# Performance work log

Measured on AMD Instinct MI355X. Metric: run time of the kernel, lower is better.

The kernel has to match this reference:

```python
import jax, jax.numpy as jnp
import numpy as np

HEADS = 8
DIM_HEAD = 64
SCALE = DIM_HEAD ** -0.5


def setup_inputs() -> dict:
    key = jax.random.key(0)
    k1, k2, k3 = jax.random.split(key, 3)
    b, p, n, dim = 2, 16, 512, 512
    inner = HEADS * DIM_HEAD  # 512
    x = jax.random.normal(k1, (b, p, n, dim), dtype=jnp.float32)
    W_qkv = jax.random.normal(k2, (dim, 3 * inner), dtype=jnp.float32) * (dim ** -0.5)
    W_out = jax.random.normal(k3, (inner, dim), dtype=jnp.float32) * (inner ** -0.5)
    b_out = jnp.zeros((dim,), dtype=jnp.float32)
    return {"x": x, "W_qkv": W_qkv, "W_out": W_out, "b_out": b_out}


def reference(x, W_qkv, W_out, b_out):
    b, p, n, dim = x.shape
    # QKV projection (no bias), split into q, k, v
    qkv = jnp.einsum('bpnd,de->bpne', x, W_qkv)
    q, k, v = jnp.split(qkv, 3, axis=-1)
    # (b, p, n, h*d) -> (b, p, h, n, d)
    def to_heads(t):
        return t.reshape(b, p, n, HEADS, DIM_HEAD).transpose(0, 1, 3, 2, 4)
    q, k, v = to_heads(q), to_heads(k), to_heads(v)
    # attention scores: (b, p, h, n, n)
    dots = jnp.einsum('bphnd,bphmd->bphnm', q, k) * SCALE
    attn = jax.nn.softmax(dots, axis=-1)
    out = jnp.einsum('bphnm,bphmd->bphnd', attn, v)
    # (b, p, h, n, d) -> (b, p, n, h*d)
    out = out.transpose(0, 1, 3, 2, 4).reshape(b, p, n, HEADS * DIM_HEAD)
    # output projection (dropout rate = 0.0 -> identity)
    return jnp.einsum('bpne,ed->bpnd', out, W_out) + b_out
```

## Files before the change

### kernel.cpp

```cpp
#include <hip/hip_runtime.h>
#include <hip/hip_bf16.h>

typedef short bf16x8 __attribute__((ext_vector_type(8)));
typedef short bf16x4 __attribute__((ext_vector_type(4)));
typedef float f32x4  __attribute__((ext_vector_type(4)));

__device__ __forceinline__ unsigned short f2bf(float f) {
    union { float fv; unsigned int u; } v; v.fv = f;
    unsigned int r = v.u + 0x7FFFu + ((v.u >> 16) & 1u);
    return (unsigned short)(r >> 16);
}

__device__ __forceinline__ void gload16(const short* g, short* l) {
    __builtin_amdgcn_global_load_lds(
        (const __attribute__((address_space(1))) void*)g,
        (__attribute__((address_space(3))) void*)l, 16, 0, 0);
}

__global__ __launch_bounds__(256) void cvt_x(
    const float* __restrict__ x, short* __restrict__ xb)
{
    size_t i = ((size_t)blockIdx.x * 256 + threadIdx.x) * 8;
    f32x4 a = *(const f32x4*)(x + i);
    f32x4 b = *(const f32x4*)(x + i + 4);
    bf16x8 s;
    #pragma unroll
    for (int e = 0; e < 4; ++e) { s[e] = (short)f2bf(a[e]); s[4 + e] = (short)f2bf(b[e]); }
    *(bf16x8*)(xb + i) = s;
}

__global__ __launch_bounds__(256) void prep_w(
    const float* __restrict__ Wqkv, const float* __restrict__ Wout,
    short* __restrict__ Wqkvt, short* __restrict__ Woutt)
{
    int idx = blockIdx.x * 256 + threadIdx.x;
    int n = idx >> 9, k = idx & 511;
    Wqkvt[idx] = (short)f2bf(Wqkv[(size_t)k * 1536 + n]);
    if (idx < 512 * 512) {
        Woutt[idx] = (short)f2bf(Wout[(size_t)k * 512 + n]);
    }
}

template<int F32OUT>
__global__ __launch_bounds__(256, 2) void gemm_db(
    const short* __restrict__ A, const short* __restrict__ Bt,
    short* __restrict__ Cb, float* __restrict__ Cf, const float* __restrict__ bias,
    int M, int N, int K, int NB)
{
    __shared__ short lds[2][2][128 * 64];
    const int t    = threadIdx.x;
    const int lane = t & 63;
    const int wid  = t >> 6;
    const int l15  = lane & 15;
    const int lg   = lane >> 4;

    const int cpx = gridDim.x >> 3;
    const int swz = (blockIdx.x & 7) * cpx + (blockIdx.x >> 3);
    const int m0 = (swz / NB) * 128;
    const int n0 = (swz % NB) * 128;

    const int wm = (wid >> 1) * 64;
    const int wn = (wid & 1) * 64;

    const int scol = 8 * ((lane & 7) ^ ((lane >> 3) & 7));

    float bval[4];
    if constexpr (F32OUT) {
        #pragma unroll
        for (int ni = 0; ni < 4; ++ni) bval[ni] = bias[n0 + wn + ni * 16 + l15];
    }

    f32x4 acc[4][4];
    #pragma unroll
    for (int i = 0; i < 4; ++i)
        #pragma unroll
        for (int j = 0; j < 4; ++j)
            acc[i][j] = f32x4{0.f, 0.f, 0.f, 0.f};

    const int NT = K >> 6;

    auto stage = [&](int buf, int tk) {
        #pragma unroll
        for (int j = 0; j < 4; ++j) {
            const int r = wid * 32 + j * 8 + (lane >> 3);
            gload16(A  + (size_t)(m0 + r) * K + tk * 64 + scol,
                    &lds[buf][0][(wid * 32 + j * 8) * 64]);
            gload16(Bt + (size_t)(n0 + r) * K + tk * 64 + scol,
                    &lds[buf][1][(wid * 32 + j * 8) * 64]);
        }
    };

    stage(0, 0);

    for (int tk = 0; tk < NT; ++tk) {
        const int cur = tk & 1;
        if (tk + 1 < NT) {
            stage(cur ^ 1, tk + 1);
            asm volatile("s_waitcnt vmcnt(8)" ::: "memory");
        } else {
            asm volatile("s_waitcnt vmcnt(0)" ::: "memory");
        }
        __builtin_amdgcn_s_barrier();

        bf16x8 af[4][2], bg[4][2];
        #pragma unroll
        for (int kk = 0; kk < 2; ++kk) {
            #pragma unroll
            for (int mi = 0; mi < 4; ++mi)
                af[mi][kk] = *(const bf16x8*)&lds[cur][0][
                    (wm + mi * 16 + l15) * 64 + (((kk * 4 + lg) ^ (l15 & 7)) * 8)];
            #pragma unroll
            for (int ni = 0; ni < 4; ++ni)
                bg[ni][kk] = *(const bf16x8*)&lds[cur][1][
                    (wn + ni * 16 + l15) * 64 + (((kk * 4 + lg) ^ (l15 & 7)) * 8)];
        }

        __builtin_amdgcn_s_setprio(1);
        #pragma unroll
        for (int kk = 0; kk < 2; ++kk)
            #pragma unroll
            for (int mi = 0; mi < 4; ++mi)
                #pragma unroll
                for (int ni = 0; ni < 4; ++ni)
                    acc[mi][ni] = __builtin_amdgcn_mfma_f32_16x16x32_bf16(
                        af[mi][kk], bg[ni][kk], acc[mi][ni], 0, 0, 0);
        __builtin_amdgcn_s_setprio(0);
        __builtin_amdgcn_s_barrier();
    }

    #pragma unroll
    for (int mi = 0; mi < 4; ++mi) {
        #pragma unroll
        for (int ni = 0; ni < 4; ++ni) {
            const int col = n0 + wn + ni * 16 + l15;
            #pragma unroll
            for (int r = 0; r < 4; ++r) {
                const int rowi = m0 + wm + mi * 16 + 4 * lg + r;
                if constexpr (F32OUT) {
                    Cf[(size_t)rowi * N + col] = acc[mi][ni][r] + bval[ni];
                } else {
                    Cb[(size_t)rowi * N + col] = (short)f2bf(acc[mi][ni][r]);
                }
            }
        }
    }
}

__global__ __launch_bounds__(512, 4) void attn_kernel(
    const short* __restrict__ qkv, short* __restrict__ attn_out)
{
    __shared__ short Kl[2][64][72];
    __shared__ short Vt[2][64][76];
    const int t    = threadIdx.x;
    const int lane = t & 63;
    const int wid  = t >> 6;
    const int l15  = lane & 15;
    const int lg   = lane >> 4;
    const int pairid = blockIdx.x & 255;
    const int qh  = blockIdx.x >> 8;
    const int bp  = pairid >> 3;
    const int h   = pairid & 7;
    const size_t tok0 = (size_t)bp * 512;
    const int q0   = qh * 256 + wid * 32;
    const int qcol = h * 64;

    bf16x8 qf[2][2];
    #pragma unroll
    for (int mj = 0; mj < 2; ++mj)
        #pragma unroll
        for (int kf = 0; kf < 2; ++kf)
            qf[mj][kf] = *(const bf16x8*)(qkv + (tok0 + q0 + mj * 16 + l15) * 1536
                                          + qcol + kf * 32 + 8 * lg);

    f32x4 ot[4][2];
    #pragma unroll
    for (int i = 0; i < 4; ++i)
        #pragma unroll
        for (int j = 0; j < 2; ++j)
            ot[i][j] = f32x4{0.f, 0.f, 0.f, 0.f};
    float mrun[2] = {-1e30f, -1e30f}, lrun[2] = {0.f, 0.f};

    const int sn = t >> 3;
    const int sd = (t & 7) * 8;

    const short* kvbase = qkv + (tok0 + sn) * 1536 + qcol + sd;
    bf16x8 kreg = *(const bf16x8*)(kvbase + 512);
    bf16x8 vreg = *(const bf16x8*)(kvbase + 1024);

    const float C = 0.18033688011112042f;

    for (int tkv = 0; tkv < 8; ++tkv) {
        const int cur = tkv & 1;
        *(bf16x8*)&Kl[cur][sn][sd] = kreg;
        #pragma unroll
        for (int i = 0; i < 8; ++i) Vt[cur][sd + i][sn] = vreg[i];
        if (tkv < 7) {
            const short* nxt = kvbase + (size_t)(tkv + 1) * 64 * 1536;
            kreg = *(const bf16x8*)(nxt + 512);
            vreg = *(const bf16x8*)(nxt + 1024);
        }
        __syncthreads();

        f32x4 st[4][2];
        #pragma unroll
        for (int i = 0; i < 4; ++i)
            #pragma unroll
            for (int j = 0; j < 2; ++j)
                st[i][j] = f32x4{0.f, 0.f, 0.f, 0.f};
        #pragma unroll
        for (int kf = 0; kf < 2; ++kf) {
            #pragma unroll
            for (int ni = 0; ni < 4; ++ni) {
                bf16x8 kfr = *(const bf16x8*)&Kl[cur][ni * 16 + l15][kf * 32 + 8 * lg];
                #pragma unroll
                for (int mj = 0; mj < 2; ++mj)
                    st[ni][mj] = __builtin_amdgcn_mfma_f32_16x16x32_bf16(
                        kfr, qf[mj][kf], st[ni][mj], 0, 0, 0);
            }
        }

        #pragma unroll
        for (int mj = 0; mj < 2; ++mj) {
            float pm = -1e30f;
            #pragma unroll
            for (int ni = 0; ni < 4; ++ni)
                #pragma unroll
                for (int r = 0; r < 4; ++r) {
                    st[ni][mj][r] *= C;
                    pm = fmaxf(pm, st[ni][mj][r]);
                }
            pm = fmaxf(pm, __shfl_xor(pm, 16));
            pm = fmaxf(pm, __shfl_xor(pm, 32));
            if (!__all(pm <= mrun[mj] + 8.f)) {
                const float mnew = fmaxf(mrun[mj], pm);
                const float fsc  = __builtin_amdgcn_exp2f(mrun[mj] - mnew);
                lrun[mj] *= fsc;
                #pragma unroll
                for (int di = 0; di < 4; ++di)
                    ot[di][mj] *= fsc;
                mrun[mj] = mnew;
            }
            float ps = 0.f;
            #pragma unroll
            for (int ni = 0; ni < 4; ++ni)
                #pragma unroll
                for (int r = 0; r < 4; ++r) {
                    float e = __builtin_amdgcn_exp2f(st[ni][mj][r] - mrun[mj]);
                    st[ni][mj][r] = e;
                    ps += e;
                }
            ps += __shfl_xor(ps, 16);
            ps += __shfl_xor(ps, 32);
            lrun[mj] += ps;
        }

        #pragma unroll
        for (int ni = 0; ni < 4; ++ni) {
            bf16x4 pb[2];
            #pragma unroll
            for (int mj = 0; mj < 2; ++mj)
                #pragma unroll
                for (int r = 0; r < 4; ++r)
                    pb[mj][r] = (short)f2bf(st[ni][mj][r]);
            #pragma unroll
            for (int di = 0; di < 4; ++di) {
                bf16x4 av = *(const bf16x4*)&Vt[cur][di * 16 + l15][ni * 16 + 4 * lg];
                #pragma unroll
                for (int mj = 0; mj < 2; ++mj)
                    ot[di][mj] = __builtin_amdgcn_mfma_f32_16x16x16bf16_1k(
                        av, pb[mj], ot[di][mj], 0, 0, 0);
            }
        }
    }

    float inv[2];
    #pragma unroll
    for (int mj = 0; mj < 2; ++mj) inv[mj] = 1.f / lrun[mj];
    #pragma unroll
    for (int di = 0; di < 4; ++di)
        #pragma unroll
        for (int mj = 0; mj < 2; ++mj) {
            const size_t tok = tok0 + q0 + mj * 16 + l15;
            const int col = qcol + di * 16 + 4 * lg;
            bf16x4 o4;
            #pragma unroll
            for (int r = 0; r < 4; ++r)
                o4[r] = (short)f2bf(ot[di][mj][r] * inv[mj]);
            *(bf16x4*)(attn_out + tok * 512 + col) = o4;
        }
}

extern "C" void kernel_launch(void* const* d_in, const int* in_sizes, int n_in,
                              void* d_out, int out_size, void* d_ws, size_t ws_size,
                              hipStream_t stream) {
    const float* x    = (const float*)d_in[0];
    const float* Wqkv = (const float*)d_in[1];
    const float* Wout = (const float*)d_in[2];
    const float* bout = (const float*)d_in[3];
    float* out = (float*)d_out;

    char* ws = (char*)d_ws;
    short* qkvb  = (short*)(ws);
    short* xb    = (short*)(ws + 50331648ull);
    short* attnb = xb;
    short* Wqkvt = (short*)(ws + 67108864ull);
    short* Woutt = (short*)(ws + 68681728ull);

    cvt_x<<<4096, 256, 0, stream>>>(x, xb);
    prep_w<<<3072, 256, 0, stream>>>(Wqkv, Wout, Wqkvt, Woutt);

    gemm_db<0><<<1536, 256, 0, stream>>>(xb, Wqkvt, qkvb, nullptr, nullptr,
                                         16384, 1536, 512, 12);

    attn_kernel<<<512, 512, 0, stream>>>(qkvb, attnb);

    gemm_db<1><<<512, 256, 0, stream>>>(attnb, Woutt, nullptr, out, bout,
                                        16384, 512, 512, 4);
}
```

Baseline: 103.3 us.

## Halve attention queries per wave, double grid, tile weight transpose

The attention kernel now gives each wave 16 queries instead of 32 and launches 1024 blocks instead of 512, which raises the number of blocks in flight and cuts per-thread register use. Each block now loads its K/V tiles for half as many queries, so K/V traffic and LDS staging per query roughly double. The softmax scale is folded into an fma ahead of exp2, MFMA sections are wrapped in s_setprio, and the bf16 conversion calls the library intrinsic. The weight prep kernel becomes an LDS-tiled transpose with coalesced reads and writes, in place of strided gathers.

```diff
diff --git a/kernel.cpp b/kernel.cpp
--- a/kernel.cpp
+++ b/kernel.cpp
@@ -9,6 +9,12 @@
     union { float fv; unsigned int u; } v; v.fv = f;
     unsigned int r = v.u + 0x7FFFu + ((v.u >> 16) & 1u);
     return (unsigned short)(r >> 16);
+}
+
+__device__ __forceinline__ short f2bf_n(float f) {
+    union { __hip_bfloat16 h; short s; } u;
+    u.h = __float2bfloat16(f);
+    return u.s;
 }
 
 __device__ __forceinline__ void gload16(const short* g, short* l) {
@@ -29,16 +35,24 @@
     *(bf16x8*)(xb + i) = s;
 }
 
-__global__ __launch_bounds__(256) void prep_w(
-    const float* __restrict__ Wqkv, const float* __restrict__ Wout,
-    short* __restrict__ Wqkvt, short* __restrict__ Woutt)
+__global__ __launch_bounds__(256) void tr_w(
+    const float* __restrict__ src, short* __restrict__ dst, int K, int N)
 {
-    int idx = blockIdx.x * 256 + threadIdx.x;
-    int n = idx >> 9, k = idx & 511;
-    Wqkvt[idx] = (short)f2bf(Wqkv[(size_t)k * 1536 + n]);
-    if (idx < 512 * 512) {
-        Woutt[idx] = (short)f2bf(Wout[(size_t)k * 512 + n]);
-    }
+    __shared__ float tile[32][33];
+    const int tx = threadIdx.x;
+    const int nb = N >> 5;
+    const int k0 = (blockIdx.x / nb) * 32;
+    const int n0 = (blockIdx.x % nb) * 32;
+    const int r  = tx >> 3;
+    const int c4 = (tx & 7) * 4;
+    f32x4 v = *(const f32x4*)(src + (size_t)(k0 + r) * N + n0 + c4);
+    #pragma unroll
+    for (int e = 0; e < 4; ++e) tile[r][c4 + e] = v[e];
+    __syncthreads();
+    bf16x4 o;
+    #pragma unroll
+    for (int e = 0; e < 4; ++e) o[e] = (short)f2bf(tile[c4 + e][r]);
+    *(bf16x4*)(dst + (size_t)(n0 + r) * K + k0 + c4) = o;
 }
 
 template<int F32OUT>
@@ -161,24 +175,19 @@
     const int bp  = pairid >> 3;
     const int h   = pairid & 7;
     const size_t tok0 = (size_t)bp * 512;
-    const int q0   = qh * 256 + wid * 32;
+    const int q0   = qh * 128 + wid * 16;
     const int qcol = h * 64;
 
-    bf16x8 qf[2][2];
-    #pragma unroll
-    for (int mj = 0; mj < 2; ++mj)
-        #pragma unroll
-        for (int kf = 0; kf < 2; ++kf)
-            qf[mj][kf] = *(const bf16x8*)(qkv + (tok0 + q0 + mj * 16 + l15) * 1536
-                                          + qcol + kf * 32 + 8 * lg);
-
-    f32x4 ot[4][2];
-    #pragma unroll
-    for (int i = 0; i < 4; ++i)
-        #pragma unroll
-        for (int j = 0; j < 2; ++j)
-            ot[i][j] = f32x4{0.f, 0.f, 0.f, 0.f};
-    float mrun[2] = {-1e30f, -1e30f}, lrun[2] = {0.f, 0.f};
+    bf16x8 qf[2];
+    #pragma unroll
+    for (int kf = 0; kf < 2; ++kf)
+        qf[kf] = *(const bf16x8*)(qkv + (tok0 + q0 + l15) * 1536
+                                  + qcol + kf * 32 + 8 * lg);
+
+    f32x4 ot[4];
+    #pragma unroll
+    for (int i = 0; i < 4; ++i) ot[i] = f32x4{0.f, 0.f, 0.f, 0.f};
+    float mrun = -1e30f, lrun = 0.f;
 
     const int sn = t >> 3;
     const int sd = (t & 7) * 8;
@@ -201,93 +210,78 @@
         }
         __syncthreads();
 
-        f32x4 st[4][2];
-        #pragma unroll
-        for (int i = 0; i < 4; ++i)
-            #pragma unroll
-            for (int j = 0; j < 2; ++j)
-                st[i][j] = f32x4{0.f, 0.f, 0.f, 0.f};
+        f32x4 st[4];
+        #pragma unroll
+        for (int i = 0; i < 4; ++i) st[i] = f32x4{0.f, 0.f, 0.f, 0.f};
+        __builtin_amdgcn_s_setprio(1);
         #pragma unroll
         for (int kf = 0; kf < 2; ++kf) {
             #pragma unroll
             for (int ni = 0; ni < 4; ++ni) {
                 bf16x8 kfr = *(const bf16x8*)&Kl[cur][ni * 16 + l15][kf * 32 + 8 * lg];
-                #pragma unroll
-                for (int mj = 0; mj < 2; ++mj)
-                    st[ni][mj] = __builtin_amdgcn_mfma_f32_16x16x32_bf16(
-                        kfr, qf[mj][kf], st[ni][mj], 0, 0, 0);
+                st[ni] = __builtin_amdgcn_mfma_f32_16x16x32_bf16(
+                    kfr, qf[kf], st[ni], 0, 0, 0);
             }
         }
-
-        #pragma unroll
-        for (int mj = 0; mj < 2; ++mj) {
-            float pm = -1e30f;
-            #pragma unroll
-            for (int ni = 0; ni < 4; ++ni)
-                #pragma unroll
-                for (int r = 0; r < 4; ++r) {
-                    st[ni][mj][r] *= C;
-                    pm = fmaxf(pm, st[ni][mj][r]);
-                }
-            pm = fmaxf(pm, __shfl_xor(pm, 16));
-            pm = fmaxf(pm, __shfl_xor(pm, 32));
-            if (!__all(pm <= mrun[mj] + 8.f)) {
-                const float mnew = fmaxf(mrun[mj], pm);
-                const float fsc  = __builtin_amdgcn_exp2f(mrun[mj] - mnew);
-                lrun[mj] *= fsc;
-                #pragma unroll
-                for (int di = 0; di < 4; ++di)
-                    ot[di][mj] *= fsc;
-                mrun[mj] = mnew;
+        __builtin_amdgcn_s_setprio(0);
+
+        float pm = -1e30f;
+        #pragma unroll
+        for (int ni = 0; ni < 4; ++ni)
+            #pragma unroll
+            for (int r = 0; r < 4; ++r)
+                pm = fmaxf(pm, st[ni][r]);
+        pm = fmaxf(pm, __shfl_xor(pm, 16));
+        pm = fmaxf(pm, __shfl_xor(pm, 32));
+        pm *= C;
+        if (!__all(pm <= mrun + 8.f)) {
+            const float mnew = fmaxf(mrun, pm);
+            const float fsc  = __builtin_amdgcn_exp2f(mrun - mnew);
+            lrun *= fsc;
+            #pragma unroll
+            for (int di = 0; di < 4; ++di) ot[di] *= fsc;
+            mrun = mnew;
+        }
+        float ps = 0.f;
+        #pragma unroll
+        for (int ni = 0; ni < 4; ++ni)
+            #pragma unroll
+            for (int r = 0; r < 4; ++r) {
+                float e = __builtin_amdgcn_exp2f(__builtin_fmaf(st[ni][r], C, -mrun));
+                st[ni][r] = e;
+                ps += e;
             }
-            float ps = 0.f;
-            #pragma unroll
-            for (int ni = 0; ni < 4; ++ni)
-                #pragma unroll
-                for (int r = 0; r < 4; ++r) {
-                    float e = __builtin_amdgcn_exp2f(st[ni][mj][r] - mrun[mj]);
-                    st[ni][mj][r] = e;
-                    ps += e;
-                }
-            ps += __shfl_xor(ps, 16);
-            ps += __shfl_xor(ps, 32);
-            lrun[mj] += ps;
-        }
-
+        ps += __shfl_xor(ps, 16);
+        ps += __shfl_xor(ps, 32);
+        lrun += ps;
+
+        __builtin_amdgcn_s_setprio(1);
         #pragma unroll
         for (int ni = 0; ni < 4; ++ni) {
-            bf16x4 pb[2];
-            #pragma unroll
-            for (int mj = 0; mj < 2; ++mj)
-                #pragma unroll
-                for (int r = 0; r < 4; ++r)
-                    pb[mj][r] = (short)f2bf(st[ni][mj][r]);
+            bf16x4 pb;
+            #pragma unroll
+            for (int r = 0; r < 4; ++r) pb[r] = f2bf_n(st[ni][r]);
             #pragma unroll
             for (int di = 0; di < 4; ++di) {
                 bf16x4 av = *(const bf16x4*)&Vt[cur][di * 16 + l15][ni * 16 + 4 * lg];
-                #pragma unroll
-                for (int mj = 0; mj < 2; ++mj)
-                    ot[di][mj] = __builtin_amdgcn_mfma_f32_16x16x16bf16_1k(
-                        av, pb[mj], ot[di][mj], 0, 0, 0);
+                ot[di] = __builtin_amdgcn_mfma_f32_16x16x16bf16_1k(
+                    av, pb, ot[di], 0, 0, 0);
             }
         }
-    }
-
-    float inv[2];
-    #pragma unroll
-    for (int mj = 0; mj < 2; ++mj) inv[mj] = 1.f / lrun[mj];
-    #pragma unroll
-    for (int di = 0; di < 4; ++di)
-        #pragma unroll
-        for (int mj = 0; mj < 2; ++mj) {
-            const size_t tok = tok0 + q0 + mj * 16 + l15;
-            const int col = qcol + di * 16 + 4 * lg;
-            bf16x4 o4;
-            #pragma unroll
-            for (int r = 0; r < 4; ++r)
-                o4[r] = (short)f2bf(ot[di][mj][r] * inv[mj]);
-            *(bf16x4*)(attn_out + tok * 512 + col) = o4;
-        }
+        __builtin_amdgcn_s_setprio(0);
+    }
+
+    const float inv = 1.f / lrun;
+    #pragma unroll
+    for (int di = 0; di < 4; ++di) {
+        const size_t tok = tok0 + q0 + l15;
+        const int col = qcol + di * 16 + 4 * lg;
+        bf16x4 o4;
+        #pragma unroll
+        for (int r = 0; r < 4; ++r)
+            o4[r] = f2bf_n(ot[di][r] * inv);
+        *(bf16x4*)(attn_out + tok * 512 + col) = o4;
+    }
 }
 
 extern "C" void kernel_launch(void* const* d_in, const int* in_sizes, int n_in,
@@ -307,12 +301,13 @@
     short* Woutt = (short*)(ws + 68681728ull);
 
     cvt_x<<<4096, 256, 0, stream>>>(x, xb);
-    prep_w<<<3072, 256, 0, stream>>>(Wqkv, Wout, Wqkvt, Woutt);
+    tr_w<<<768, 256, 0, stream>>>(Wqkv, Wqkvt, 512, 1536);
+    tr_w<<<256, 256, 0, stream>>>(Wout, Woutt, 512, 512);
 
     gemm_db<0><<<1536, 256, 0, stream>>>(xb, Wqkvt, qkvb, nullptr, nullptr,
                                          16384, 1536, 512, 12);
 
-    attn_kernel<<<512, 512, 0, stream>>>(qkvb, attnb);
+    attn_kernel<<<1024, 512, 0, stream>>>(qkvb, attnb);
 
     gemm_db<1><<<512, 256, 0, stream>>>(attnb, Woutt, nullptr, out, bout,
                                         16384, 512, 512, 4);
```

Measured after the change: 103.4 us. No clear change (+0.1%).
